# Kernel optimization log

Hardware: AMD Instinct MI355X
Metric: run time of the kernel (lower is better)

The kernel has to match this reference:

```python
import jax, jax.numpy as jnp
import numpy as np

# NTU RGB+D skeleton parent connectivity (from the original module's self.conn)
CONN = np.array([0, 0, 1, 2, 0, 4, 5, 3, 6, 9, 9, 12, 24, 11, 12,
                 13, 14, 15, 16, 15, 16, 15, 16, 11, 23], dtype=np.int32)


def setup_inputs() -> dict:
    key = jax.random.key(0)
    N, C, T, V, M = 128, 3, 300, 25, 2
    x = jax.random.normal(key, (N, C, T, V, M), dtype=jnp.float32)
    conn = jnp.asarray(CONN)
    return {"x": x, "conn": conn}


def reference(x, conn):
    # x: (N, C, T, V, M). Faithful vectorization of EfficientGCN.preprocess.
    N, C, T, V, M = x.shape
    eps = jnp.asarray(1e-4, x.dtype)

    # --- joint branch: [x ; x - x_center] where center joint index = 1 ---
    rel = x - x[:, :, :, 1:2, :]                      # (N,C,T,V,M)
    joint = jnp.concatenate([x, rel], axis=1)         # (N,2C,T,V,M)

    # --- velocity branch: 1-step and 2-step finite differences,
    #     filled for frames 0..T-3, last two frames are zero ---
    zeros2 = jnp.zeros((N, C, 2, V, M), dtype=x.dtype)
    v1 = jnp.concatenate([x[:, :, 1:T-1] - x[:, :, 0:T-2], zeros2], axis=2)
    v2 = jnp.concatenate([x[:, :, 2:T] - x[:, :, 0:T-2], zeros2], axis=2)
    velocity = jnp.concatenate([v1, v2], axis=1)      # (N,2C,T,V,M)

    # --- bone branch: joint - parent(joint), plus per-axis angle via acos ---
    bone_vec = x - x[:, :, :, conn, :]                # (N,C,T,V,M) gather along V
    bone_length = jnp.sqrt(jnp.sum(bone_vec * bone_vec, axis=1, keepdims=True)) + eps
    bone_ang = jnp.arccos(bone_vec / bone_length)     # (N,C,T,V,M)
    bone = jnp.concatenate([bone_vec, bone_ang], axis=1)  # (N,2C,T,V,M)

    # stack branches: (N, 3, 2C, T, V, M)
    return jnp.stack([joint, velocity, bone], axis=1)
```

## Files before the change

kernel.cpp:

```cpp
#include <hip/hip_runtime.h>
#include <math.h>


#define NN 128
#define CC 3
#define TT 300
#define VV 25
#define MM 2

constexpr int TVM  = TT * VV * MM;
constexpr int TV   = TT * VV;
constexpr int OUTP = 3 * 6 * TVM;

__global__ __launch_bounds__(256)
void egcn_pre_kernel(const float* __restrict__ x,
                     const int* __restrict__ conn,
                     float* __restrict__ out) {
    int j = blockIdx.x * blockDim.x + threadIdx.x;
    if (j >= NN * TV) return;

    int n  = j / TV;
    int rv = j - n * TV;
    int t  = rv / VV;
    int v  = rv - t * VV;

    int pv = conn[v];
    bool hasvel = (t < TT - 2);

    const float* xn = x + (size_t)n * CC * TVM;

    float2 xv[3], xc[3], xp[3], x1[3], x2[3];
    #pragma unroll
    for (int c = 0; c < 3; ++c) {
        const float2* p2 = reinterpret_cast<const float2*>(xn + c * TVM);
        xv[c] = p2[rv];
        xc[c] = p2[t * VV + 1];
        xp[c] = p2[t * VV + pv];
        if (hasvel) {
            x1[c] = p2[rv + VV];
            x2[c] = p2[rv + 2 * VV];
        } else {
            x1[c] = make_float2(0.f, 0.f);
            x2[c] = make_float2(0.f, 0.f);
        }
    }

    float2 bv[3];
    float ss0 = 0.f, ss1 = 0.f;
    #pragma unroll
    for (int c = 0; c < 3; ++c) {
        bv[c].x = xv[c].x - xp[c].x;
        bv[c].y = xv[c].y - xp[c].y;
        ss0 += bv[c].x * bv[c].x;
        ss1 += bv[c].y * bv[c].y;
    }
    float inv0 = 1.0f / (sqrtf(ss0) + 1e-4f);
    float inv1 = 1.0f / (sqrtf(ss1) + 1e-4f);

    float2* outn = reinterpret_cast<float2*>(out + (size_t)n * OUTP);

    #pragma unroll
    for (int c = 0; c < 3; ++c) {
        float2 rel = make_float2(xv[c].x - xc[c].x, xv[c].y - xc[c].y);
        outn[(0 * 6 + c)     * TV + rv] = xv[c];
        outn[(0 * 6 + c + 3) * TV + rv] = rel;

        float2 v1 = hasvel ? make_float2(x1[c].x - xv[c].x, x1[c].y - xv[c].y)
                           : make_float2(0.f, 0.f);
        float2 v2 = hasvel ? make_float2(x2[c].x - xv[c].x, x2[c].y - xv[c].y)
                           : make_float2(0.f, 0.f);
        outn[(1 * 6 + c)     * TV + rv] = v1;
        outn[(1 * 6 + c + 3) * TV + rv] = v2;

        float2 ang = make_float2(acosf(bv[c].x * inv0), acosf(bv[c].y * inv1));
        outn[(2 * 6 + c)     * TV + rv] = bv[c];
        outn[(2 * 6 + c + 3) * TV + rv] = ang;
    }
}

extern "C" void kernel_launch(void* const* d_in, const int* in_sizes, int n_in,
                              void* d_out, int out_size, void* d_ws, size_t ws_size,
                              hipStream_t stream) {
    const float* x   = (const float*)d_in[0];
    const int* conn  = (const int*)d_in[1];
    float* out       = (float*)d_out;

    int total = NN * TV;
    int block = 256;
    int grid  = (total + block - 1) / block;
    egcn_pre_kernel<<<grid, block, 0, stream>>>(x, conn, out);
}
```

Before: 162.9 us.

## Process four floats per thread with 16-byte loads and nontemporal stores

Each thread now handles four consecutive elements of a plane instead of one (v,m) pair, giving 16-byte vector loads and stores. Output stores use nontemporal hints to avoid polluting cache on a write-heavy kernel. Center and parent loads become scalar gathers with per-element index math, and velocity zeroing uses a multiply mask. The bounds check is removed, which relies on the element count dividing evenly by the block size.

```diff
diff --git a/kernel.cpp b/kernel.cpp
--- a/kernel.cpp
+++ b/kernel.cpp
@@ -2,91 +2,101 @@
 #include <math.h>
 
 
-#define NN 128
-#define CC 3
-#define TT 300
-#define VV 25
-#define MM 2
+typedef float vfloat4 __attribute__((ext_vector_type(4)));
+typedef float vfloat2 __attribute__((ext_vector_type(2)));
 
-constexpr int TVM  = TT * VV * MM;
-constexpr int TV   = TT * VV;
-constexpr int OUTP = 3 * 6 * TVM;
+constexpr int PLANE = 15000;
+constexpr int QPN   = PLANE / 4;
+constexpr int NQ    = 128 * QPN;
 
 __global__ __launch_bounds__(256)
 void egcn_pre_kernel(const float* __restrict__ x,
                      const int* __restrict__ conn,
                      float* __restrict__ out) {
-    int j = blockIdx.x * blockDim.x + threadIdx.x;
-    if (j >= NN * TV) return;
+    int q = blockIdx.x * blockDim.x + threadIdx.x;
+    int n = q / QPN;
+    int f = (q - n * QPN) << 2;
 
-    int n  = j / TV;
-    int rv = j - n * TV;
-    int t  = rv / VV;
-    int v  = rv - t * VV;
+    int idxc[4], idxp[4];
+    float vmask[4];
+#pragma unroll
+    for (int i = 0; i < 4; ++i) {
+        int e  = f + i;
+        int ti = e / 50;
+        int vm = e - ti * 50;
+        int mi = vm & 1;
+        idxc[i]  = ti * 50 + 2 + mi;
+        idxp[i]  = ti * 50 + (conn[vm >> 1] << 1) + mi;
+        vmask[i] = (ti < 298) ? 1.0f : 0.0f;
+    }
+    const bool anyvel = (f < 14900);
 
-    int pv = conn[v];
-    bool hasvel = (t < TT - 2);
-
-    const float* xn = x + (size_t)n * CC * TVM;
-
-    float2 xv[3], xc[3], xp[3], x1[3], x2[3];
-    #pragma unroll
+    const float* xn = x + (size_t)n * (3 * PLANE);
+    float xv[3][4], x1[3][4], x2[3][4], xc[3][4], xp[3][4];
+#pragma unroll
     for (int c = 0; c < 3; ++c) {
-        const float2* p2 = reinterpret_cast<const float2*>(xn + c * TVM);
-        xv[c] = p2[rv];
-        xc[c] = p2[t * VV + 1];
-        xp[c] = p2[t * VV + pv];
-        if (hasvel) {
-            x1[c] = p2[rv + VV];
-            x2[c] = p2[rv + 2 * VV];
+        const float* pl = xn + c * PLANE;
+        *reinterpret_cast<vfloat4*>(xv[c]) = *reinterpret_cast<const vfloat4*>(pl + f);
+        if (anyvel) {
+            *reinterpret_cast<vfloat2*>(&x1[c][0]) = *reinterpret_cast<const vfloat2*>(pl + f + 50);
+            *reinterpret_cast<vfloat2*>(&x1[c][2]) = *reinterpret_cast<const vfloat2*>(pl + f + 52);
+            *reinterpret_cast<vfloat2*>(&x2[c][0]) = *reinterpret_cast<const vfloat2*>(pl + f + 100);
+            *reinterpret_cast<vfloat2*>(&x2[c][2]) = *reinterpret_cast<const vfloat2*>(pl + f + 102);
         } else {
-            x1[c] = make_float2(0.f, 0.f);
-            x2[c] = make_float2(0.f, 0.f);
+#pragma unroll
+            for (int i = 0; i < 4; ++i) { x1[c][i] = 0.f; x2[c][i] = 0.f; }
+        }
+#pragma unroll
+        for (int i = 0; i < 4; ++i) {
+            xc[c][i] = pl[idxc[i]];
+            xp[c][i] = pl[idxp[i]];
         }
     }
 
-    float2 bv[3];
-    float ss0 = 0.f, ss1 = 0.f;
-    #pragma unroll
+    float inv[4];
+#pragma unroll
+    for (int i = 0; i < 4; ++i) {
+        float b0 = xv[0][i] - xp[0][i];
+        float b1 = xv[1][i] - xp[1][i];
+        float b2 = xv[2][i] - xp[2][i];
+        inv[i] = 1.0f / (sqrtf(b0 * b0 + b1 * b1 + b2 * b2) + 1e-4f);
+    }
+
+    float* outn = out + (size_t)n * (18 * PLANE);
+    auto st = [&](int plane, float a, float b, float c2, float d) {
+        vfloat4 val = {a, b, c2, d};
+        __builtin_nontemporal_store(val,
+            reinterpret_cast<vfloat4*>(outn + plane * PLANE + f));
+    };
+
+#pragma unroll
     for (int c = 0; c < 3; ++c) {
-        bv[c].x = xv[c].x - xp[c].x;
-        bv[c].y = xv[c].y - xp[c].y;
-        ss0 += bv[c].x * bv[c].x;
-        ss1 += bv[c].y * bv[c].y;
-    }
-    float inv0 = 1.0f / (sqrtf(ss0) + 1e-4f);
-    float inv1 = 1.0f / (sqrtf(ss1) + 1e-4f);
-
-    float2* outn = reinterpret_cast<float2*>(out + (size_t)n * OUTP);
-
-    #pragma unroll
-    for (int c = 0; c < 3; ++c) {
-        float2 rel = make_float2(xv[c].x - xc[c].x, xv[c].y - xc[c].y);
-        outn[(0 * 6 + c)     * TV + rv] = xv[c];
-        outn[(0 * 6 + c + 3) * TV + rv] = rel;
-
-        float2 v1 = hasvel ? make_float2(x1[c].x - xv[c].x, x1[c].y - xv[c].y)
-                           : make_float2(0.f, 0.f);
-        float2 v2 = hasvel ? make_float2(x2[c].x - xv[c].x, x2[c].y - xv[c].y)
-                           : make_float2(0.f, 0.f);
-        outn[(1 * 6 + c)     * TV + rv] = v1;
-        outn[(1 * 6 + c + 3) * TV + rv] = v2;
-
-        float2 ang = make_float2(acosf(bv[c].x * inv0), acosf(bv[c].y * inv1));
-        outn[(2 * 6 + c)     * TV + rv] = bv[c];
-        outn[(2 * 6 + c + 3) * TV + rv] = ang;
+        st(c,     xv[c][0], xv[c][1], xv[c][2], xv[c][3]);
+        st(c + 3, xv[c][0] - xc[c][0], xv[c][1] - xc[c][1],
+                  xv[c][2] - xc[c][2], xv[c][3] - xc[c][3]);
+        st(c + 6, (x1[c][0] - xv[c][0]) * vmask[0], (x1[c][1] - xv[c][1]) * vmask[1],
+                  (x1[c][2] - xv[c][2]) * vmask[2], (x1[c][3] - xv[c][3]) * vmask[3]);
+        st(c + 9, (x2[c][0] - xv[c][0]) * vmask[0], (x2[c][1] - xv[c][1]) * vmask[1],
+                  (x2[c][2] - xv[c][2]) * vmask[2], (x2[c][3] - xv[c][3]) * vmask[3]);
+        float bv[4], ang[4];
+#pragma unroll
+        for (int i = 0; i < 4; ++i) {
+            bv[i]  = xv[c][i] - xp[c][i];
+            ang[i] = acosf(bv[i] * inv[i]);
+        }
+        st(c + 12, bv[0], bv[1], bv[2], bv[3]);
+        st(c + 15, ang[0], ang[1], ang[2], ang[3]);
     }
 }
 
 extern "C" void kernel_launch(void* const* d_in, const int* in_sizes, int n_in,
                               void* d_out, int out_size, void* d_ws, size_t ws_size,
                               hipStream_t stream) {
-    const float* x   = (const float*)d_in[0];
-    const int* conn  = (const int*)d_in[1];
-    float* out       = (float*)d_out;
+    const float* x  = (const float*)d_in[0];
+    const int* conn = (const int*)d_in[1];
+    float* out      = (float*)d_out;
 
-    int total = NN * TV;
     int block = 256;
-    int grid  = (total + block - 1) / block;
+    int grid  = NQ / block;
     egcn_pre_kernel<<<grid, block, 0, stream>>>(x, conn, out);
 }
```

Result: no change. 164.7 us (+1.1%).
